# Optimization experiments

Measured on AMD Instinct MI355X. Metric: run time of the kernel, lower is better.

## Reference

```python
import jax, jax.numpy as jnp
import numpy as np

B, S, D_MODEL, D_HEAD = 4, 4096, 512, 64


def setup_inputs() -> dict:
    key = jax.random.key(0)
    ks = jax.random.split(key, 9)
    s = 1.0 / np.sqrt(D_MODEL)
    return {
        "q_in": jax.random.normal(ks[0], (B, S, D_MODEL), jnp.float32),
        "k_in": jax.random.normal(ks[1], (B, S, D_MODEL), jnp.float32),
        "v_in": jax.random.normal(ks[2], (B, S, D_MODEL), jnp.float32),
        "Wq": jax.random.normal(ks[3], (D_HEAD, D_MODEL), jnp.float32) * s,
        "bq": jax.random.normal(ks[4], (D_HEAD,), jnp.float32) * s,
        "Wk": jax.random.normal(ks[5], (D_HEAD, D_MODEL), jnp.float32) * s,
        "bk": jax.random.normal(ks[6], (D_HEAD,), jnp.float32) * s,
        "Wv": jax.random.normal(ks[7], (D_HEAD, D_MODEL), jnp.float32) * s,
        "bv": jax.random.normal(ks[8], (D_HEAD,), jnp.float32) * s,
    }


def reference(q_in, k_in, v_in, Wq, bq, Wk, bk, Wv, bv):
    # Linear projections (torch nn.Linear: x @ W.T + b)
    q = jnp.einsum("bsd,hd->bsh", q_in, Wq) + bq  # [B,S,Dh]
    k = jnp.einsum("bsd,hd->bsh", k_in, Wk) + bk
    v = jnp.einsum("bsd,hd->bsh", v_in, Wv) + bv
    # Causal mask: -inf strictly above diagonal (generate_attention_mask, triu(1))
    sk = k.shape[1]
    mask = jnp.triu(jnp.full((q.shape[1], sk), -jnp.inf, dtype=q.dtype), k=1)
    scores = jnp.einsum("bqh,bkh->bqk", q, k) / jnp.sqrt(jnp.asarray(q.shape[-1], q.dtype))
    attn = jax.nn.softmax(scores + mask, axis=-1)  # [B,S,S]
    return jnp.einsum("bqk,bkh->bqh", attn, v)
```

## Files before the change

kernel.cpp:

```cpp
#include <hip/hip_runtime.h>
#include <hip/hip_bf16.h>

#define B_ 4
#define S_ 4096
#define DM 512
#define DH 64

#define NEG_BIG (-3.0e38f)
#define MCLAMP  (-1.0e30f)

typedef __attribute__((ext_vector_type(8))) short short8b;
typedef __attribute__((ext_vector_type(4))) float f32x4;

__device__ __forceinline__ f32x4 MFMA16(short8b a, short8b b, f32x4 c) {
    return __builtin_amdgcn_mfma_f32_16x16x32_bf16(a, b, c, 0, 0, 0);
}

__device__ __forceinline__ float bf2f(unsigned short u) {
    unsigned int x = ((unsigned int)u) << 16;
    float f;
    __builtin_memcpy(&f, &x, 4);
    return f;
}
__device__ __forceinline__ unsigned short f2bf_rne(float f) {
    unsigned int u = __float_as_uint(f);
    u += 0x7FFFu + ((u >> 16) & 1u);
    return (unsigned short)(u >> 16);
}

__device__ __forceinline__ void gload16(const void* gp, void* lp) {
    __builtin_amdgcn_global_load_lds(
        (const __attribute__((address_space(1))) void*)gp,
        (__attribute__((address_space(3))) void*)lp, 16, 0, 0);
}

__global__ void detect_kernel(const unsigned short* __restrict__ u,
                              int* __restrict__ flag) {
    __shared__ int cnt;
    if (threadIdx.x == 0) cnt = 0;
    __syncthreads();
    int w = 0;
    #pragma unroll
    for (int k = 0; k < 8; ++k) {
        unsigned short x = u[threadIdx.x * 8 + k];
        int e = (x >> 7) & 0xFF;
        if (e >= 135 || (e > 0 && e <= 95)) ++w;
    }
    atomicAdd(&cnt, w);
    __syncthreads();
    if (threadIdx.x == 0) *flag = (cnt > 64) ? 1 : 0;
}

#define TM 64
#define KC 64
#define LDX 68
#define LDW 65

__global__ __launch_bounds__(256) void proj_kernel(
    const void* __restrict__ xq, const void* __restrict__ xk,
    const void* __restrict__ xv,
    const void* __restrict__ Wq, const void* __restrict__ Wk,
    const void* __restrict__ Wv,
    const void* __restrict__ bq, const void* __restrict__ bk,
    const void* __restrict__ bv,
    unsigned short* __restrict__ Qhp, unsigned short* __restrict__ Qlp,
    unsigned short* __restrict__ Khp, unsigned short* __restrict__ Klp,
    unsigned short* __restrict__ Vthp, unsigned short* __restrict__ Vtlp,
    const int* __restrict__ flag)
{
    const int which = blockIdx.y;
    const void* x    = (which == 0) ? xq : (which == 1) ? xk : xv;
    const void* W    = (which == 0) ? Wq : (which == 1) ? Wk : Wv;
    const void* bias = (which == 0) ? bq : (which == 1) ? bk : bv;

    const bool f32 = (*flag != 0);
    const int row0 = blockIdx.x * TM;
    const int t    = threadIdx.x;
    const int tr   = t >> 4;
    const int tc   = t & 15;

    __shared__ float Xs[TM][LDX];
    __shared__ float Ws[KC][LDW];

    float acc[4][4];
    #pragma unroll
    for (int r = 0; r < 4; ++r)
        #pragma unroll
        for (int h = 0; h < 4; ++h) acc[r][h] = 0.f;

    for (int kc = 0; kc < DM; kc += KC) {
        __syncthreads();
        if (f32) {
            const float* xb = (const float*)x;
            #pragma unroll
            for (int jv = 0; jv < 4; ++jv) {
                int lidx = jv * 256 + t;
                int r = lidx >> 4, kq = lidx & 15;
                float4 v = *reinterpret_cast<const float4*>(
                    xb + (size_t)(row0 + r) * DM + kc + kq * 4);
                *reinterpret_cast<float4*>(&Xs[r][kq * 4]) = v;
            }
            const float* wb = (const float*)W;
            #pragma unroll
            for (int jv = 0; jv < 4; ++jv) {
                int lidx = jv * 256 + t;
                int h = lidx >> 4, kq = lidx & 15;
                float4 v = *reinterpret_cast<const float4*>(
                    wb + (size_t)h * DM + kc + kq * 4);
                Ws[kq * 4 + 0][h] = v.x;
                Ws[kq * 4 + 1][h] = v.y;
                Ws[kq * 4 + 2][h] = v.z;
                Ws[kq * 4 + 3][h] = v.w;
            }
        } else {
            const unsigned short* xb = (const unsigned short*)x;
            #pragma unroll
            for (int jv = 0; jv < 4; ++jv) {
                int lidx = jv * 256 + t;
                int r = lidx >> 4, kq = lidx & 15;
                ushort4 u = *reinterpret_cast<const ushort4*>(
                    xb + (size_t)(row0 + r) * DM + kc + kq * 4);
                Xs[r][kq * 4 + 0] = bf2f(u.x);
                Xs[r][kq * 4 + 1] = bf2f(u.y);
                Xs[r][kq * 4 + 2] = bf2f(u.z);
                Xs[r][kq * 4 + 3] = bf2f(u.w);
            }
            const unsigned short* wb = (const unsigned short*)W;
            #pragma unroll
            for (int jv = 0; jv < 4; ++jv) {
                int lidx = jv * 256 + t;
                int h = lidx >> 4, kq = lidx & 15;
                ushort4 u = *reinterpret_cast<const ushort4*>(
                    wb + (size_t)h * DM + kc + kq * 4);
                Ws[kq * 4 + 0][h] = bf2f(u.x);
                Ws[kq * 4 + 1][h] = bf2f(u.y);
                Ws[kq * 4 + 2][h] = bf2f(u.z);
                Ws[kq * 4 + 3][h] = bf2f(u.w);
            }
        }
        __syncthreads();

        #pragma unroll
        for (int k4 = 0; k4 < KC / 4; ++k4) {
            float4 xv4[4], wv4[4];
            #pragma unroll
            for (int r = 0; r < 4; ++r)
                xv4[r] = *reinterpret_cast<const float4*>(&Xs[tr * 4 + r][k4 * 4]);
            #pragma unroll
            for (int j = 0; j < 4; ++j)
                wv4[j] = *reinterpret_cast<const float4*>(&Ws[k4 * 4 + j][tc * 4]);
            #pragma unroll
            for (int r = 0; r < 4; ++r) {
                const float* xp = reinterpret_cast<const float*>(&xv4[r]);
                #pragma unroll
                for (int j = 0; j < 4; ++j) {
                    const float* wp = reinterpret_cast<const float*>(&wv4[j]);
                    float xs = xp[j];
                    #pragma unroll
                    for (int h = 0; h < 4; ++h)
                        acc[r][h] = fmaf(xs, wp[h], acc[r][h]);
                }
            }
        }
    }

    float bs[4];
    #pragma unroll
    for (int h = 0; h < 4; ++h)
        bs[h] = f32 ? ((const float*)bias)[tc * 4 + h]
                    : bf2f(((const unsigned short*)bias)[tc * 4 + h]);

    if (which < 2) {
        unsigned short* ph = (which == 0) ? Qhp : Khp;
        unsigned short* pl = (which == 0) ? Qlp : Klp;
        const float scale = (which == 0) ? 0.125f : 1.0f;
        #pragma unroll
        for (int r = 0; r < 4; ++r) {
            ushort4 h4, l4v;
            unsigned short* hp = (unsigned short*)&h4;
            unsigned short* lp = (unsigned short*)&l4v;
            #pragma unroll
            for (int h = 0; h < 4; ++h) {
                float v = (acc[r][h] + bs[h]) * scale;
                unsigned short hb = f2bf_rne(v);
                hp[h] = hb;
                lp[h] = f2bf_rne(v - bf2f(hb));
            }
            const size_t off = (size_t)(row0 + tr * 4 + r) * DH + tc * 4;
            *reinterpret_cast<ushort4*>(ph + off) = h4;
            *reinterpret_cast<ushort4*>(pl + off) = l4v;
        }
    } else {
        const int bb = row0 >> 12;
        const int s0 = row0 & 4095;
        #pragma unroll
        for (int j = 0; j < 4; ++j) {
            ushort4 h4, l4v;
            unsigned short* hp = (unsigned short*)&h4;
            unsigned short* lp = (unsigned short*)&l4v;
            #pragma unroll
            for (int r = 0; r < 4; ++r) {
                float v = acc[r][j] + bs[j];
                unsigned short hb = f2bf_rne(v);
                hp[r] = hb;
                lp[r] = f2bf_rne(v - bf2f(hb));
            }
            const size_t off = (size_t)(bb * 64 + tc * 4 + j) * S_ + s0 + tr * 4;
            *reinterpret_cast<ushort4*>(Vthp + off) = h4;
            *reinterpret_cast<ushort4*>(Vtlp + off) = l4v;
        }
    }
}

__global__ __launch_bounds__(512, 2) void flash_kernel(
    const unsigned short* __restrict__ Qh, const unsigned short* __restrict__ Ql,
    const unsigned short* __restrict__ Kh, const unsigned short* __restrict__ Kl,
    const unsigned short* __restrict__ Vth, const unsigned short* __restrict__ Vtl,
    void* __restrict__ out, const int* __restrict__ flag)
{
    const int pair = blockIdx.x;
    const int b    = blockIdx.y;
    const int t    = threadIdx.x;
    const int lane = t & 63;
    const int w    = t >> 6;
    const int qh   = w & 1;
    const int kh   = w >> 1;
    const int l15  = lane & 15;
    const int l4   = lane >> 4;

    __shared__ __align__(16) char smem[8192 + 2 * 65536];
    __shared__ float Mg[4][32];
    __shared__ float Lg[4][32];
    __shared__ float Ltot[32];

    const size_t bS = (size_t)b * S_;
    const bool f32o = (*flag != 0);

    const int qp   = t >> 8;
    const int qrow = (t & 255) >> 3;
    const int qsg  = t & 7;

    const int klaneoff = ((lane >> 3) << 7) +
                         ((((lane & 7) << 4)) ^ ((lane >> 3) << 4));
    const int vrl = lane >> 4;
    const int voff0 = (vrl << 13) + ((((lane & 15) << 4)) ^ (vrl << 4));
    const int voff1 = (vrl << 13) + ((((lane & 15) << 4)) ^ ((4 + vrl) << 4));

    const char* Khb = (const char*)Kh + bS * 128;
    const char* Klb = (const char*)Kl + bS * 128;
    const char* Vhb = (const char*)Vth + (size_t)b * 64 * 8192;
    const char* Vlb = (const char*)Vtl + (size_t)b * 64 * 8192;

    auto issue_tile = [&](int kt, int bsel) {
        char* buf = smem + 8192 + bsel * 65536;
        if (w < 4) {
            #pragma unroll
            for (int j = 0; j < 8; ++j) {
                const int c2  = w * 8 + j;
                const int p   = c2 >> 4;
                const int ckp = c2 & 15;
                const char* g = (p ? Klb : Khb) +
                                (size_t)kt * 16384 + ckp * 1024 + klaneoff;
                gload16(g, buf + p * 16384 + ckp * 1024);
            }
        } else {
            #pragma unroll
            for (int j = 0; j < 8; ++j) {
                const int c2  = (w - 4) * 8 + j;
                const int p   = c2 >> 4;
                const int cvp = c2 & 15;
                const int vo  = (cvp & 1) ? voff1 : voff0;
                const char* g = (p ? Vlb : Vhb) +
                                (size_t)cvp * 32768 + (size_t)kt * 256 + vo;
                gload16(g, buf + 32768 + p * 16384 + cvp * 1024);
            }
        }
    };

    #pragma unroll 1
    for (int hf = 0; hf < 2; ++hf) {
        const int qt = hf ? (127 - pair) : pair;
        const int q0 = qt << 5;
        const int nk = (qt >> 2) + 1;

        __syncthreads();

        {
            const unsigned short* src = qp ? Ql : Qh;
            uint4 v = *reinterpret_cast<const uint4*>(
                src + (bS + q0 + qrow) * 64 + qsg * 8);
            const int off = qp * 4096 + qrow * 128 +
                            ((qsg * 16) ^ ((qrow & 7) << 4));
            *reinterpret_cast<uint4*>(smem + off) = v;
        }
        issue_tile(0, 0);
        __syncthreads();

        short8b qf[2][2];
        #pragma unroll
        for (int p = 0; p < 2; ++p)
            #pragma unroll
            for (int ks = 0; ks < 2; ++ks) {
                const int row = qh * 16 + l15;
                const int off = p * 4096 + row * 128 +
                                ((ks * 64 + l4 * 16) ^ ((row & 7) << 4));
                qf[p][ks] = *reinterpret_cast<const short8b*>(smem + off);
            }
        __syncthreads();

        f32x4 of[4];
        of[0] = f32x4{0.f, 0.f, 0.f, 0.f};
        of[1] = f32x4{0.f, 0.f, 0.f, 0.f};
        of[2] = f32x4{0.f, 0.f, 0.f, 0.f};
        of[3] = f32x4{0.f, 0.f, 0.f, 0.f};
        float mrun[4], lrun[4];
        #pragma unroll
        for (int r = 0; r < 4; ++r) { mrun[r] = NEG_BIG; lrun[r] = 0.f; }

        #pragma unroll 1
        for (int kt = 0; kt < nk; ++kt) {
            const int bsel = kt & 1;
            if (kt + 1 < nk) issue_tile(kt + 1, bsel ^ 1);

            const char* kb = smem + 8192 + bsel * 65536;
            const char* vb = kb + 32768;

            f32x4 sc[2];
            #pragma unroll
            for (int ct = 0; ct < 2; ++ct) {
                f32x4 a = f32x4{0.f, 0.f, 0.f, 0.f};
                #pragma unroll
                for (int ks = 0; ks < 2; ++ks) {
                    const int row = kh * 32 + ct * 16 + l15;
                    const int off = row * 128 +
                                    ((ks * 64 + l4 * 16) ^ ((row & 7) << 4));
                    short8b bh = *reinterpret_cast<const short8b*>(kb + off);
                    short8b bl = *reinterpret_cast<const short8b*>(kb + 16384 + off);
                    a = MFMA16(qf[1][ks], bh, a);
                    a = MFMA16(qf[0][ks], bl, a);
                    a = MFMA16(qf[0][ks], bh, a);
                }
                sc[ct] = a;
            }

            if (kt == nk - 1) {
                #pragma unroll
                for (int ct = 0; ct < 2; ++ct) {
                    const int col = kt * 128 + kh * 32 + ct * 16 + l15;
                    #pragma unroll
                    for (int r = 0; r < 4; ++r) {
                        const int row = q0 + qh * 16 + l4 * 4 + r;
                        if (col > row) sc[ct][r] = NEG_BIG;
                    }
                }
            }

            float pm[4];
            #pragma unroll
            for (int r = 0; r < 4; ++r) pm[r] = fmaxf(sc[0][r], sc[1][r]);
            #pragma unroll
            for (int s = 1; s < 16; s <<= 1)
                #pragma unroll
                for (int r = 0; r < 4; ++r)
                    pm[r] = fmaxf(pm[r], __shfl_xor(pm[r], s));

            float alpha[4], ps[4];
            #pragma unroll
            for (int r = 0; r < 4; ++r) {
                const float mn = fmaxf(fmaxf(mrun[r], pm[r]), MCLAMP);
                alpha[r] = __expf(mrun[r] - mn);
                mrun[r] = mn;
                sc[0][r] = __expf(sc[0][r] - mn);
                sc[1][r] = __expf(sc[1][r] - mn);
                ps[r] = sc[0][r] + sc[1][r];
            }
            #pragma unroll
            for (int s = 1; s < 16; s <<= 1)
                #pragma unroll
                for (int r = 0; r < 4; ++r) ps[r] += __shfl_xor(ps[r], s);
            #pragma unroll
            for (int r = 0; r < 4; ++r) lrun[r] = lrun[r] * alpha[r] + ps[r];
            #pragma unroll
            for (int c = 0; c < 4; ++c)
                #pragma unroll
                for (int r = 0; r < 4; ++r) of[c][r] *= alpha[r];

            #pragma unroll
            for (int ct = 0; ct < 2; ++ct)
                #pragma unroll
                for (int r = 0; r < 4; ++r) {
                    const int row = qh * 16 + l4 * 4 + r;
                    const int col = kh * 32 + ct * 16 + l15;
                    const int off = row * 256 + ((col * 2) ^ ((row & 7) << 4));
                    *reinterpret_cast<unsigned short*>(smem + off) =
                        f2bf_rne(sc[ct][r]);
                }
            asm volatile("s_waitcnt lgkmcnt(0)" ::: "memory");
            __builtin_amdgcn_sched_barrier(0);

            short8b pf;
            {
                const int row = qh * 16 + l15;
                const int off = row * 256 + ((kh * 64 + l4 * 16) ^ ((row & 7) << 4));
                pf = *reinterpret_cast<const short8b*>(smem + off);
            }
            #pragma unroll
            for (int ct = 0; ct < 4; ++ct) {
                const int vr = ct * 16 + l15;
                const int voff = vr * 256 +
                                 ((kh * 64 + l4 * 16) ^ ((vr & 7) << 4));
                short8b vh = *reinterpret_cast<const short8b*>(vb + voff);
                short8b vl = *reinterpret_cast<const short8b*>(vb + 16384 + voff);
                of[ct] = MFMA16(pf, vl, of[ct]);
                of[ct] = MFMA16(pf, vh, of[ct]);
            }

            __syncthreads();
        }

        if (l15 == 0) {
            #pragma unroll
            for (int r = 0; r < 4; ++r) {
                const int row = qh * 16 + l4 * 4 + r;
                Mg[kh][row] = mrun[r];
                Lg[kh][row] = lrun[r];
            }
        }
        __syncthreads();

        float* Op = reinterpret_cast<float*>(smem + 8192);
        #pragma unroll
        for (int r = 0; r < 4; ++r) {
            const int row = qh * 16 + l4 * 4 + r;
            const float M = fmaxf(fmaxf(Mg[0][row], Mg[1][row]),
                                  fmaxf(Mg[2][row], Mg[3][row]));
            const float L = Lg[0][row] * __expf(Mg[0][row] - M)
                          + Lg[1][row] * __expf(Mg[1][row] - M)
                          + Lg[2][row] * __expf(Mg[2][row] - M)
                          + Lg[3][row] * __expf(Mg[3][row] - M);
            const float al = __expf(mrun[r] - M);
            #pragma unroll
            for (int c = 0; c < 4; ++c)
                Op[kh * 2048 + row * 64 + c * 16 + l15] = of[c][r] * al;
            if (kh == 0 && l15 == 0) Ltot[row] = L;
        }
        __syncthreads();

        {
            const int row = t >> 4;
            const int d0  = (t & 15) << 2;
            float4 s = {0.f, 0.f, 0.f, 0.f};
            #pragma unroll
            for (int g = 0; g < 4; ++g) {
                float4 v = *reinterpret_cast<const float4*>(
                    Op + g * 2048 + row * 64 + d0);
                s.x += v.x; s.y += v.y; s.z += v.z; s.w += v.w;
            }
            const float inv = 1.0f / Ltot[row];
            const size_t oi = (bS + q0 + row) * 64 + d0;
            if (f32o) {
                float4 o;
                o.x = s.x * inv; o.y = s.y * inv;
                o.z = s.z * inv; o.w = s.w * inv;
                *reinterpret_cast<float4*>((float*)out + oi) = o;
            } else {
                ushort4 o;
                o.x = f2bf_rne(s.x * inv);
                o.y = f2bf_rne(s.y * inv);
                o.z = f2bf_rne(s.z * inv);
                o.w = f2bf_rne(s.w * inv);
                *reinterpret_cast<ushort4*>((unsigned short*)out + oi) = o;
            }
        }
    }
}

extern "C" void kernel_launch(void* const* d_in, const int* in_sizes, int n_in,
                              void* d_out, int out_size, void* d_ws, size_t ws_size,
                              hipStream_t stream) {
    const size_t NP = (size_t)B_ * S_ * DH;
    unsigned short* Qhp  = (unsigned short*)d_ws;
    unsigned short* Qlp  = Qhp + NP;
    unsigned short* Khp  = Qhp + 2 * NP;
    unsigned short* Klp  = Qhp + 3 * NP;
    unsigned short* Vthp = Qhp + 4 * NP;
    unsigned short* Vtlp = Qhp + 5 * NP;
    int* flag = (int*)(Qhp + 6 * NP);

    detect_kernel<<<1, 256, 0, stream>>>((const unsigned short*)d_in[0], flag);

    proj_kernel<<<dim3(B_ * S_ / TM, 3), 256, 0, stream>>>(
        d_in[0], d_in[1], d_in[2],
        d_in[3], d_in[5], d_in[7],
        d_in[4], d_in[6], d_in[8],
        Qhp, Qlp, Khp, Klp, Vthp, Vtlp, flag);

    flash_kernel<<<dim3(64, B_), 512, 0, stream>>>(
        Qhp, Qlp, Khp, Klp, Vthp, Vtlp, d_out, flag);
}
```

Before: 247.1 us.

## Rewrite projection GEMM with split-bf16 MFMA and swizzled LDS staging

The scalar FP32 FMA projection GEMM is replaced by bf16 MFMA 16x16x32 instructions. Both the X and W tiles are split into high and low bf16 parts and combined with three MFMAs to approximate FP32 accuracy. Tiles are staged in XOR-swizzled shared memory, and the epilogue goes through an LDS transpose so global stores are coalesced 16-byte writes, including the transposed V output. The aim is to cut the projection stage's compute time, at the cost of a slight precision change from the 3-term bf16 split and extra conversion work during staging.

```diff
diff --git a/kernel.cpp b/kernel.cpp
--- a/kernel.cpp
+++ b/kernel.cpp
@@ -26,6 +26,9 @@
     unsigned int u = __float_as_uint(f);
     u += 0x7FFFu + ((u >> 16) & 1u);
     return (unsigned short)(u >> 16);
+}
+__device__ __forceinline__ unsigned int pk2(unsigned short a, unsigned short b) {
+    return (unsigned int)a | ((unsigned int)b << 16);
 }
 
 __device__ __forceinline__ void gload16(const void* gp, void* lp) {
@@ -51,10 +54,8 @@
     if (threadIdx.x == 0) *flag = (cnt > 64) ? 1 : 0;
 }
 
-#define TM 64
-#define KC 64
-#define LDX 68
-#define LDW 65
+#define PM 64
+#define PK 64
 
 __global__ __launch_bounds__(256) void proj_kernel(
     const void* __restrict__ xq, const void* __restrict__ xk,
@@ -74,140 +75,166 @@
     const void* bias = (which == 0) ? bq : (which == 1) ? bk : bv;
 
     const bool f32 = (*flag != 0);
-    const int row0 = blockIdx.x * TM;
+    const int row0 = blockIdx.x * PM;
     const int t    = threadIdx.x;
-    const int tr   = t >> 4;
-    const int tc   = t & 15;
-
-    __shared__ float Xs[TM][LDX];
-    __shared__ float Ws[KC][LDW];
-
-    float acc[4][4];
+    const int lane = t & 63;
+    const int w    = t >> 6;
+    const int l15  = lane & 15;
+    const int l4   = lane >> 4;
+
+    __shared__ __align__(16) char sm[32768];
+
+    const int srow = t >> 2;
+    const int sseg = t & 3;
+    const int swz  = (srow & 7) << 4;
+
+    f32x4 acc[4];
     #pragma unroll
-    for (int r = 0; r < 4; ++r)
-        #pragma unroll
-        for (int h = 0; h < 4; ++h) acc[r][h] = 0.f;
-
-    for (int kc = 0; kc < DM; kc += KC) {
-        __syncthreads();
+    for (int n = 0; n < 4; ++n) acc[n] = f32x4{0.f, 0.f, 0.f, 0.f};
+
+    #pragma unroll 1
+    for (int kc = 0; kc < DM / PK; ++kc) {
+        const int k0 = kc * PK;
+        __syncthreads();
+
         if (f32) {
-            const float* xb = (const float*)x;
-            #pragma unroll
-            for (int jv = 0; jv < 4; ++jv) {
-                int lidx = jv * 256 + t;
-                int r = lidx >> 4, kq = lidx & 15;
-                float4 v = *reinterpret_cast<const float4*>(
-                    xb + (size_t)(row0 + r) * DM + kc + kq * 4);
-                *reinterpret_cast<float4*>(&Xs[r][kq * 4]) = v;
-            }
-            const float* wb = (const float*)W;
-            #pragma unroll
-            for (int jv = 0; jv < 4; ++jv) {
-                int lidx = jv * 256 + t;
-                int h = lidx >> 4, kq = lidx & 15;
-                float4 v = *reinterpret_cast<const float4*>(
-                    wb + (size_t)h * DM + kc + kq * 4);
-                Ws[kq * 4 + 0][h] = v.x;
-                Ws[kq * 4 + 1][h] = v.y;
-                Ws[kq * 4 + 2][h] = v.z;
-                Ws[kq * 4 + 3][h] = v.w;
+            #pragma unroll
+            for (int m = 0; m < 2; ++m) {
+                const float* p = (m == 0)
+                    ? (const float*)x + (size_t)(row0 + srow) * DM + k0 + sseg * 16
+                    : (const float*)W + (size_t)srow * DM + k0 + sseg * 16;
+                float v[16];
+                #pragma unroll
+                for (int j = 0; j < 4; ++j) {
+                    float4 f = *reinterpret_cast<const float4*>(p + j * 4);
+                    v[j * 4 + 0] = f.x; v[j * 4 + 1] = f.y;
+                    v[j * 4 + 2] = f.z; v[j * 4 + 3] = f.w;
+                }
+                unsigned short hh[16], ll[16];
+                #pragma unroll
+                for (int j = 0; j < 16; ++j) {
+                    unsigned short hb = f2bf_rne(v[j]);
+                    hh[j] = hb;
+                    ll[j] = f2bf_rne(v[j] - bf2f(hb));
+                }
+                char* dh = sm + m * 16384 + srow * 128;
+                char* dl = dh + 8192;
+                #pragma unroll
+                for (int g = 0; g < 2; ++g) {
+                    const int off = (sseg * 32 + g * 16) ^ swz;
+                    uint4 hu, lu;
+                    hu.x = pk2(hh[g*8+0], hh[g*8+1]); hu.y = pk2(hh[g*8+2], hh[g*8+3]);
+                    hu.z = pk2(hh[g*8+4], hh[g*8+5]); hu.w = pk2(hh[g*8+6], hh[g*8+7]);
+                    lu.x = pk2(ll[g*8+0], ll[g*8+1]); lu.y = pk2(ll[g*8+2], ll[g*8+3]);
+                    lu.z = pk2(ll[g*8+4], ll[g*8+5]); lu.w = pk2(ll[g*8+6], ll[g*8+7]);
+                    *reinterpret_cast<uint4*>(dh + off) = hu;
+                    *reinterpret_cast<uint4*>(dl + off) = lu;
+                }
             }
         } else {
-            const unsigned short* xb = (const unsigned short*)x;
-            #pragma unroll
-            for (int jv = 0; jv < 4; ++jv) {
-                int lidx = jv * 256 + t;
-                int r = lidx >> 4, kq = lidx & 15;
-                ushort4 u = *reinterpret_cast<const ushort4*>(
-                    xb + (size_t)(row0 + r) * DM + kc + kq * 4);
-                Xs[r][kq * 4 + 0] = bf2f(u.x);
-                Xs[r][kq * 4 + 1] = bf2f(u.y);
-                Xs[r][kq * 4 + 2] = bf2f(u.z);
-                Xs[r][kq * 4 + 3] = bf2f(u.w);
-            }
-            const unsigned short* wb = (const unsigned short*)W;
-            #pragma unroll
-            for (int jv = 0; jv < 4; ++jv) {
-                int lidx = jv * 256 + t;
-                int h = lidx >> 4, kq = lidx & 15;
-                ushort4 u = *reinterpret_cast<const ushort4*>(
-                    wb + (size_t)h * DM + kc + kq * 4);
-                Ws[kq * 4 + 0][h] = bf2f(u.x);
-                Ws[kq * 4 + 1][h] = bf2f(u.y);
-                Ws[kq * 4 + 2][h] = bf2f(u.z);
-                Ws[kq * 4 + 3][h] = bf2f(u.w);
-            }
-        }
-        __syncthreads();
-
-        #pragma unroll
-        for (int k4 = 0; k4 < KC / 4; ++k4) {
-            float4 xv4[4], wv4[4];
-            #pragma unroll
-            for (int r = 0; r < 4; ++r)
-                xv4[r] = *reinterpret_cast<const float4*>(&Xs[tr * 4 + r][k4 * 4]);
-            #pragma unroll
-            for (int j = 0; j < 4; ++j)
-                wv4[j] = *reinterpret_cast<const float4*>(&Ws[k4 * 4 + j][tc * 4]);
-            #pragma unroll
-            for (int r = 0; r < 4; ++r) {
-                const float* xp = reinterpret_cast<const float*>(&xv4[r]);
-                #pragma unroll
-                for (int j = 0; j < 4; ++j) {
-                    const float* wp = reinterpret_cast<const float*>(&wv4[j]);
-                    float xs = xp[j];
-                    #pragma unroll
-                    for (int h = 0; h < 4; ++h)
-                        acc[r][h] = fmaf(xs, wp[h], acc[r][h]);
-                }
+            const uint4 z = {0u, 0u, 0u, 0u};
+            #pragma unroll
+            for (int m = 0; m < 2; ++m) {
+                const unsigned short* p = (m == 0)
+                    ? (const unsigned short*)x + (size_t)(row0 + srow) * DM + k0 + sseg * 16
+                    : (const unsigned short*)W + (size_t)srow * DM + k0 + sseg * 16;
+                char* dh = sm + m * 16384 + srow * 128;
+                char* dl = dh + 8192;
+                #pragma unroll
+                for (int g = 0; g < 2; ++g) {
+                    uint4 hv = *reinterpret_cast<const uint4*>(p + g * 8);
+                    const int off = (sseg * 32 + g * 16) ^ swz;
+                    *reinterpret_cast<uint4*>(dh + off) = hv;
+                    *reinterpret_cast<uint4*>(dl + off) = z;
+                }
+            }
+        }
+        __syncthreads();
+
+        const int arow = w * 16 + l15;
+        short8b xh[2], xl[2];
+        #pragma unroll
+        for (int ks = 0; ks < 2; ++ks) {
+            const int off = arow * 128 + ((ks * 64 + l4 * 16) ^ ((arow & 7) << 4));
+            xh[ks] = *reinterpret_cast<const short8b*>(sm + off);
+            xl[ks] = *reinterpret_cast<const short8b*>(sm + 8192 + off);
+        }
+        #pragma unroll
+        for (int n = 0; n < 4; ++n) {
+            #pragma unroll
+            for (int ks = 0; ks < 2; ++ks) {
+                const int brow = n * 16 + l15;
+                const int off = brow * 128 + ((ks * 64 + l4 * 16) ^ ((brow & 7) << 4));
+                short8b wh = *reinterpret_cast<const short8b*>(sm + 16384 + off);
+                short8b wl = *reinterpret_cast<const short8b*>(sm + 24576 + off);
+                acc[n] = MFMA16(xh[ks], wl, acc[n]);
+                acc[n] = MFMA16(xl[ks], wh, acc[n]);
+                acc[n] = MFMA16(xh[ks], wh, acc[n]);
             }
         }
     }
 
-    float bs[4];
+    __syncthreads();
+    float* C = reinterpret_cast<float*>(sm);
     #pragma unroll
-    for (int h = 0; h < 4; ++h)
-        bs[h] = f32 ? ((const float*)bias)[tc * 4 + h]
-                    : bf2f(((const unsigned short*)bias)[tc * 4 + h]);
+    for (int n = 0; n < 4; ++n)
+        #pragma unroll
+        for (int r = 0; r < 4; ++r)
+            C[(w * 16 + l4 * 4 + r) * 66 + n * 16 + l15] = acc[n][r];
+    __syncthreads();
 
     if (which < 2) {
         unsigned short* ph = (which == 0) ? Qhp : Khp;
         unsigned short* pl = (which == 0) ? Qlp : Klp;
         const float scale = (which == 0) ? 0.125f : 1.0f;
-        #pragma unroll
-        for (int r = 0; r < 4; ++r) {
-            ushort4 h4, l4v;
-            unsigned short* hp = (unsigned short*)&h4;
-            unsigned short* lp = (unsigned short*)&l4v;
-            #pragma unroll
-            for (int h = 0; h < 4; ++h) {
-                float v = (acc[r][h] + bs[h]) * scale;
-                unsigned short hb = f2bf_rne(v);
-                hp[h] = hb;
-                lp[h] = f2bf_rne(v - bf2f(hb));
-            }
-            const size_t off = (size_t)(row0 + tr * 4 + r) * DH + tc * 4;
-            *reinterpret_cast<ushort4*>(ph + off) = h4;
-            *reinterpret_cast<ushort4*>(pl + off) = l4v;
+        const int r_  = t >> 2;
+        const int c0_ = (t & 3) * 16;
+        unsigned short hh[16], ll[16];
+        #pragma unroll
+        for (int j = 0; j < 16; ++j) {
+            const float bv_ = f32 ? ((const float*)bias)[c0_ + j]
+                                  : bf2f(((const unsigned short*)bias)[c0_ + j]);
+            const float v = (C[r_ * 66 + c0_ + j] + bv_) * scale;
+            unsigned short hb = f2bf_rne(v);
+            hh[j] = hb;
+            ll[j] = f2bf_rne(v - bf2f(hb));
+        }
+        const size_t off = (size_t)(row0 + r_) * DH + c0_;
+        #pragma unroll
+        for (int g = 0; g < 2; ++g) {
+            uint4 hu, lu;
+            hu.x = pk2(hh[g*8+0], hh[g*8+1]); hu.y = pk2(hh[g*8+2], hh[g*8+3]);
+            hu.z = pk2(hh[g*8+4], hh[g*8+5]); hu.w = pk2(hh[g*8+6], hh[g*8+7]);
+            lu.x = pk2(ll[g*8+0], ll[g*8+1]); lu.y = pk2(ll[g*8+2], ll[g*8+3]);
+            lu.z = pk2(ll[g*8+4], ll[g*8+5]); lu.w = pk2(ll[g*8+6], ll[g*8+7]);
+            *reinterpret_cast<uint4*>(ph + off + g * 8) = hu;
+            *reinterpret_cast<uint4*>(pl + off + g * 8) = lu;
         }
     } else {
+        const int c_ = t & 63;
+        const int rb = (t >> 6) * 16;
         const int bb = row0 >> 12;
-        const int s0 = row0 & 4095;
-        #pragma unroll
-        for (int j = 0; j < 4; ++j) {
-            ushort4 h4, l4v;
-            unsigned short* hp = (unsigned short*)&h4;
-            unsigned short* lp = (unsigned short*)&l4v;
-            #pragma unroll
-            for (int r = 0; r < 4; ++r) {
-                float v = acc[r][j] + bs[j];
-                unsigned short hb = f2bf_rne(v);
-                hp[r] = hb;
-                lp[r] = f2bf_rne(v - bf2f(hb));
-            }
-            const size_t off = (size_t)(bb * 64 + tc * 4 + j) * S_ + s0 + tr * 4;
-            *reinterpret_cast<ushort4*>(Vthp + off) = h4;
-            *reinterpret_cast<ushort4*>(Vtlp + off) = l4v;
+        const int s0 = row0 & (S_ - 1);
+        const float bv_ = f32 ? ((const float*)bias)[c_]
+                              : bf2f(((const unsigned short*)bias)[c_]);
+        unsigned short hh[16], ll[16];
+        #pragma unroll
+        for (int i = 0; i < 16; ++i) {
+            const float v = C[(rb + i) * 66 + c_] + bv_;
+            unsigned short hb = f2bf_rne(v);
+            hh[i] = hb;
+            ll[i] = f2bf_rne(v - bf2f(hb));
+        }
+        const size_t off = (size_t)(bb * 64 + c_) * S_ + s0 + rb;
+        #pragma unroll
+        for (int g = 0; g < 2; ++g) {
+            uint4 hu, lu;
+            hu.x = pk2(hh[g*8+0], hh[g*8+1]); hu.y = pk2(hh[g*8+2], hh[g*8+3]);
+            hu.z = pk2(hh[g*8+4], hh[g*8+5]); hu.w = pk2(hh[g*8+6], hh[g*8+7]);
+            lu.x = pk2(ll[g*8+0], ll[g*8+1]); lu.y = pk2(ll[g*8+2], ll[g*8+3]);
+            lu.z = pk2(ll[g*8+4], ll[g*8+5]); lu.w = pk2(ll[g*8+6], ll[g*8+7]);
+            *reinterpret_cast<uint4*>(Vthp + off + g * 8) = hu;
+            *reinterpret_cast<uint4*>(Vtlp + off + g * 8) = lu;
         }
     }
 }
@@ -489,7 +516,7 @@
 
     detect_kernel<<<1, 256, 0, stream>>>((const unsigned short*)d_in[0], flag);
 
-    proj_kernel<<<dim3(B_ * S_ / TM, 3), 256, 0, stream>>>(
+    proj_kernel<<<dim3(B_ * S_ / PM, 3), 256, 0, stream>>>(
         d_in[0], d_in[1], d_in[2],
         d_in[3], d_in[5], d_in[7],
         d_in[4], d_in[6], d_in[8],
```

After: 220.0 us. 1.12x faster.
